# Performance work log

Measured on AMD Instinct MI355X. Metric: run time of the kernel, lower is better.

## Reference

```python
import jax, jax.numpy as jnp
import numpy as np

EMB, HEADS = 1024, 16
HEAD_DIM = EMB // HEADS


def _linear(x, W, b):
    # torch nn.Linear convention: x @ W.T + b, W: [out, in]
    return jnp.einsum('bse,oe->bso', x, W) + b


def setup_inputs() -> dict:
    key = jax.random.key(0)
    ks = jax.random.split(key, 11)
    B, S = 2, 2048
    sc = 1.0 / np.sqrt(EMB)
    inp = {
        'x': jax.random.normal(ks[0], (B, S, EMB), dtype=jnp.float32),
        'y': jax.random.normal(ks[1], (B, S, EMB), dtype=jnp.float32),
        'mask': jnp.ones((B, S, S), dtype=jnp.int32),
        'Wq': jax.random.normal(ks[2], (EMB, EMB), dtype=jnp.float32) * sc,
        'bq': jax.random.normal(ks[3], (EMB,), dtype=jnp.float32) * sc,
        'Wk': jax.random.normal(ks[4], (EMB, EMB), dtype=jnp.float32) * sc,
        'bk': jax.random.normal(ks[5], (EMB,), dtype=jnp.float32) * sc,
        'Wv': jax.random.normal(ks[6], (EMB, EMB), dtype=jnp.float32) * sc,
        'bv': jax.random.normal(ks[7], (EMB,), dtype=jnp.float32) * sc,
        'Wo': jax.random.normal(ks[8], (EMB, EMB), dtype=jnp.float32) * sc,
        'bo': jax.random.normal(ks[9], (EMB,), dtype=jnp.float32) * sc,
    }
    return inp


def reference(x, y, mask, Wq, bq, Wk, bk, Wv, bv, Wo, bo):
    B, S, _ = x.shape
    q = _linear(x, Wq, bq).reshape(B, S, HEADS, HEAD_DIM).transpose(0, 2, 1, 3)
    k = _linear(y, Wk, bk).reshape(B, -1, HEADS, HEAD_DIM).transpose(0, 2, 1, 3)
    v = _linear(y, Wv, bv).reshape(B, -1, HEADS, HEAD_DIM).transpose(0, 2, 1, 3)
    # scores: [B, H, Sq, Sk]
    score = jnp.einsum('bhqd,bhkd->bhqk', q, k) / jnp.sqrt(jnp.float32(HEAD_DIM))
    # NOTE: original torch code calls score.masked_fill(...) without assignment,
    # so the mask has no effect on the computation (faithfully ignored here).
    weights = jax.nn.softmax(score, axis=-1)
    attn = jnp.einsum('bhqk,bhkd->bhqd', weights, v)
    attn = attn.transpose(0, 2, 1, 3).reshape(B, S, EMB)
    # dropout is identity in eval mode
    return _linear(attn, Wo, bo)
```

## Files before the change

kernel.cpp:

```cpp
#include <hip/hip_runtime.h>
#include <cstdint>
#include <cstddef>

#define BB 2
#define SS 2048
#define EE 1024
#define HH 16
#define DD 64

typedef __attribute__((ext_vector_type(8))) short short8;
typedef __attribute__((ext_vector_type(4))) short shortx4;
typedef __attribute__((ext_vector_type(8))) unsigned short ushort8;
typedef __attribute__((ext_vector_type(4))) unsigned short ush4;
typedef __attribute__((ext_vector_type(4))) float floatx4;

#define MFMA32(a, b, c) __builtin_amdgcn_mfma_f32_16x16x32_bf16((a), (b), (c), 0, 0, 0)
#define MFMA16(a, b, c) __builtin_amdgcn_mfma_f32_16x16x16bf16_1k((a), (b), (c), 0, 0, 0)

#define QSCALE 0.18033688011112042f

#define G2L16(g, l)                                                        \
    __builtin_amdgcn_global_load_lds(                                      \
        (const __attribute__((address_space(1))) void*)(g),                \
        (__attribute__((address_space(3))) void*)(l), 16, 0, 0)

__device__ __forceinline__ unsigned short f2bf(float f) {
    unsigned int u = __float_as_uint(f);
    u += 0x7fffu + ((u >> 16) & 1u);
    return (unsigned short)(u >> 16);
}

__device__ __forceinline__ unsigned int pkbf(float a, float b) {
    return __builtin_amdgcn_perm(__float_as_uint(b) + 0x8000u,
                                 __float_as_uint(a) + 0x8000u, 0x07060302u);
}

__global__ __launch_bounds__(256) void k_cvt(
    const float* __restrict__ x, unsigned short* __restrict__ xb,
    const float* __restrict__ y, unsigned short* __restrict__ yb,
    const float* __restrict__ w0, unsigned short* __restrict__ d0,
    const float* __restrict__ w1, unsigned short* __restrict__ d1,
    const float* __restrict__ w2, unsigned short* __restrict__ d2,
    const float* __restrict__ w3, unsigned short* __restrict__ d3)
{
    const int g = blockIdx.y;
    if (g >= 2 && blockIdx.x >= 256) return;
    const float* s = (g == 0) ? x : (g == 1) ? y : (g == 2) ? w0
                   : (g == 3) ? w1 : (g == 4) ? w2 : w3;
    unsigned short* d = (g == 0) ? xb : (g == 1) ? yb : (g == 2) ? d0
                      : (g == 3) ? d1 : (g == 4) ? d2 : d3;
    const size_t i = ((size_t)blockIdx.x * 256 + threadIdx.x) * 16;
    floatx4 f0 = *(const floatx4*)(s + i);
    floatx4 f1 = *(const floatx4*)(s + i + 4);
    floatx4 f2 = *(const floatx4*)(s + i + 8);
    floatx4 f3 = *(const floatx4*)(s + i + 12);
    ushort8 o0, o1;
#pragma unroll
    for (int j = 0; j < 4; ++j) { o0[j] = f2bf(f0[j]); o0[j + 4] = f2bf(f1[j]); }
#pragma unroll
    for (int j = 0; j < 4; ++j) { o1[j] = f2bf(f2[j]); o1[j + 4] = f2bf(f3[j]); }
    *(ushort8*)(d + i) = o0;
    *(ushort8*)(d + i + 8) = o1;
}

template <int MT, int OMODE>
__device__ __forceinline__ void gemm_body(
    const unsigned short* __restrict__ A, const unsigned short* __restrict__ W,
    const float* __restrict__ bias, void* __restrict__ Cv, float oscale,
    int m0, int n0, unsigned short* As0, unsigned short* As1,
    unsigned short* Bs0, unsigned short* Bs1)
{
    constexpr int K = 1024, N = 1024, LDT = 32;
    constexpr int MFR = MT / 32;
    const int t = threadIdx.x;
    const int lane = t & 63, w = t >> 6;
    const int q = lane >> 4, c = lane & 15;
    const int wm = w & 1, wn = w >> 1;
    const int lr = lane >> 2, lc = (lane & 3) * 8;

    const unsigned short* gA0 = A + (size_t)(m0 + w * (MT / 4) + lr) * K + lc;
    const unsigned short* gA1 = gA0 + 16 * K;
    unsigned short* lA0_0 = As0 + (w * (MT / 4)) * LDT;
    unsigned short* lA0_1 = lA0_0 + 16 * LDT;
    unsigned short* lA1_0 = As1 + (w * (MT / 4)) * LDT;
    unsigned short* lA1_1 = lA1_0 + 16 * LDT;
    const unsigned short* gB0 = W + (size_t)(n0 + w * 32 + lr) * K + lc;
    const unsigned short* gB1 = gB0 + 16 * K;
    unsigned short* lB0_0 = Bs0 + (w * 32) * LDT;
    unsigned short* lB0_1 = lB0_0 + 16 * LDT;
    unsigned short* lB1_0 = Bs1 + (w * 32) * LDT;
    unsigned short* lB1_1 = lB1_0 + 16 * LDT;

    floatx4 acc[MFR][4] = {};

    for (int kt = 0; kt < K; kt += 64) {
        __syncthreads();
        G2L16(gA0 + kt, lA0_0);
        if constexpr (MT == 128) G2L16(gA1 + kt, lA0_1);
        G2L16(gA0 + kt + 32, lA1_0);
        if constexpr (MT == 128) G2L16(gA1 + kt + 32, lA1_1);
        G2L16(gB0 + kt, lB0_0);
        G2L16(gB1 + kt, lB0_1);
        G2L16(gB0 + kt + 32, lB1_0);
        G2L16(gB1 + kt + 32, lB1_1);
        __syncthreads();

        const unsigned short* Ah[2] = {As0, As1};
        const unsigned short* Bh[2] = {Bs0, Bs1};
#pragma unroll
        for (int hf = 0; hf < 2; ++hf) {
            short8 af[MFR], bfr[4];
#pragma unroll
            for (int mi = 0; mi < MFR; ++mi)
                af[mi] = *(const short8*)
                    &Ah[hf][(wm * (MFR * 16) + mi * 16 + c) * LDT + q * 8];
#pragma unroll
            for (int ni = 0; ni < 4; ++ni)
                bfr[ni] = *(const short8*)
                    &Bh[hf][(wn * 64 + ni * 16 + c) * LDT + q * 8];
#pragma unroll
            for (int mi = 0; mi < MFR; ++mi)
#pragma unroll
                for (int ni = 0; ni < 4; ++ni)
                    acc[mi][ni] = MFMA32(af[mi], bfr[ni], acc[mi][ni]);
        }
    }

#pragma unroll
    for (int ni = 0; ni < 4; ++ni) {
        const int col = n0 + wn * 64 + ni * 16 + c;
        const float bv = bias[col];
#pragma unroll
        for (int mi = 0; mi < MFR; ++mi)
#pragma unroll
            for (int r = 0; r < 4; ++r) {
                const int row = m0 + wm * (MFR * 16) + mi * 16 + q * 4 + r;
                const float v = (acc[mi][ni][r] + bv) * oscale;
                if constexpr (OMODE == 0) {
                    ((unsigned short*)Cv)[(size_t)row * N + col] = f2bf(v);
                } else if constexpr (OMODE == 1) {
                    const int b = row >> 11, s = row & 2047;
                    ((unsigned short*)Cv)[((size_t)(b * 1024 + col)) * SS + s] = f2bf(v);
                } else {
                    ((float*)Cv)[(size_t)row * N + col] = v;
                }
            }
    }
}

__global__ __launch_bounds__(256) void k_gemm_qkv(
    const unsigned short* __restrict__ x, const unsigned short* __restrict__ y,
    const unsigned short* __restrict__ Wq, const float* __restrict__ bq,
    const unsigned short* __restrict__ Wk, const float* __restrict__ bk,
    const unsigned short* __restrict__ Wv, const float* __restrict__ bv,
    unsigned short* __restrict__ Q, unsigned short* __restrict__ Ko,
    unsigned short* __restrict__ Vt)
{
    __shared__ __align__(16) unsigned short As0[128 * 32], As1[128 * 32];
    __shared__ __align__(16) unsigned short Bs0[128 * 32], Bs1[128 * 32];
    const int m0 = blockIdx.y * 128;
    const int nt = blockIdx.x;
    const int g = nt >> 3;
    const int n0 = (nt & 7) * 128;
    if (g == 0) {
        gemm_body<128, 0>(x, Wq, bq, Q, QSCALE, m0, n0, As0, As1, Bs0, Bs1);
    } else if (g == 1) {
        gemm_body<128, 0>(y, Wk, bk, Ko, 1.0f, m0, n0, As0, As1, Bs0, Bs1);
    } else {
        gemm_body<128, 1>(y, Wv, bv, Vt, 1.0f, m0, n0, As0, As1, Bs0, Bs1);
    }
}

__global__ __launch_bounds__(256) void k_gemm_out(
    const unsigned short* __restrict__ A, const unsigned short* __restrict__ W,
    const float* __restrict__ bias, float* __restrict__ C)
{
    __shared__ __align__(16) unsigned short As0[64 * 32], As1[64 * 32];
    __shared__ __align__(16) unsigned short Bs0[128 * 32], Bs1[128 * 32];
    gemm_body<64, 2>(A, W, bias, C, 1.0f, blockIdx.y * 64, blockIdx.x * 128,
                     As0, As1, Bs0, Bs1);
}

__global__ __launch_bounds__(256, 2) void k_attn(
    const unsigned short* __restrict__ Q, const unsigned short* __restrict__ K,
    const unsigned short* __restrict__ Vt, unsigned short* __restrict__ O)
{
    constexpr int LDK = 72;
    __shared__ __align__(16) unsigned short Ks[64 * LDK];
    __shared__ __align__(16) unsigned short Vs[64 * 64];

    const int bh = blockIdx.x, qt = blockIdx.y;
    const int b = bh >> 4, h = bh & 15;
    const int t = threadIdx.x, w = t >> 6;
    const int lane = t & 63, q = lane >> 4, c = lane & 15;

    short8 qb[2][2];
#pragma unroll
    for (int g = 0; g < 2; ++g) {
        const size_t qoff =
            (size_t)(b * SS + qt * 128 + w * 32 + g * 16 + c) * EE + h * DD + q * 8;
        qb[g][0] = *(const short8*)(Q + qoff);
        qb[g][1] = *(const short8*)(Q + qoff + 32);
    }

    floatx4 o[2][4] = {};
    floatx4 lacc[2] = {};
    const shortx4 ones = {(short)0x3F80, (short)0x3F80, (short)0x3F80, (short)0x3F80};

    const int sr = t >> 2, sp = (t & 3) * 16;
    const int vkey = (sr & 15) << 2;
    const unsigned short* Kg = K + (size_t)(b * SS + sr) * EE + h * DD + sp;
    const unsigned short* Vg = Vt + ((size_t)bh * DD + sr) * SS + sp;

    for (int kt = 0; kt < SS; kt += 64) {
        __syncthreads();
        {
            const ushort8* gk = (const ushort8*)(Kg + (size_t)kt * EE);
            ushort8 k0 = gk[0], k1 = gk[1];
            *(ushort8*)&Ks[sr * LDK + sp] = k0;
            *(ushort8*)&Ks[sr * LDK + sp + 8] = k1;
            const ushort8* gv = (const ushort8*)(Vg + kt);
            ushort8 v0 = gv[0], v1 = gv[1];
            *(ush4*)&Vs[sr * 64 + ((sp +  0) ^ vkey)] =
                __builtin_shufflevector(v0, v0, 0, 1, 2, 3);
            *(ush4*)&Vs[sr * 64 + ((sp +  4) ^ vkey)] =
                __builtin_shufflevector(v0, v0, 4, 5, 6, 7);
            *(ush4*)&Vs[sr * 64 + ((sp +  8) ^ vkey)] =
                __builtin_shufflevector(v1, v1, 0, 1, 2, 3);
            *(ush4*)&Vs[sr * 64 + ((sp + 12) ^ vkey)] =
                __builtin_shufflevector(v1, v1, 4, 5, 6, 7);
        }
        __syncthreads();

        shortx4 pa[2][4];
#pragma unroll
        for (int tt = 0; tt < 4; ++tt) {
            const short8 ka0 = *(const short8*)&Ks[(tt * 16 + c) * LDK + q * 8];
            const short8 ka1 = *(const short8*)&Ks[(tt * 16 + c) * LDK + 32 + q * 8];
#pragma unroll
            for (int g = 0; g < 2; ++g) {
                floatx4 s = {0.f, 0.f, 0.f, 0.f};
                s = MFMA32(ka0, qb[g][0], s);
                s = MFMA32(ka1, qb[g][1], s);
                union { unsigned int u[2]; shortx4 v; } pk;
                pk.u[0] = pkbf(exp2f(s[0]), exp2f(s[1]));
                pk.u[1] = pkbf(exp2f(s[2]), exp2f(s[3]));
                pa[g][tt] = pk.v;
            }
        }

#pragma unroll
        for (int nd = 0; nd < 4; ++nd)
#pragma unroll
            for (int tt = 0; tt < 4; ++tt) {
                const shortx4 vb = *(const shortx4*)
                    &Vs[(nd * 16 + c) * 64 + (((tt * 4 + q) ^ c) << 2)];
                o[0][nd] = MFMA16(pa[0][tt], vb, o[0][nd]);
                o[1][nd] = MFMA16(pa[1][tt], vb, o[1][nd]);
            }
#pragma unroll
        for (int tt = 0; tt < 4; ++tt) {
            lacc[0] = MFMA16(pa[0][tt], ones, lacc[0]);
            lacc[1] = MFMA16(pa[1][tt], ones, lacc[1]);
        }
    }

#pragma unroll
    for (int g = 0; g < 2; ++g) {
        float linv[4];
#pragma unroll
        for (int r = 0; r < 4; ++r) linv[r] = __builtin_amdgcn_rcpf(lacc[g][r]);
        const int orow = b * SS + qt * 128 + w * 32 + g * 16;
#pragma unroll
        for (int nd = 0; nd < 4; ++nd)
#pragma unroll
            for (int r = 0; r < 4; ++r)
                O[(size_t)(orow + q * 4 + r) * EE + h * DD + nd * 16 + c] =
                    f2bf(o[g][nd][r] * linv[r]);
    }
}

extern "C" void kernel_launch(void* const* d_in, const int* in_sizes, int n_in,
                              void* d_out, int out_size, void* d_ws, size_t ws_size,
                              hipStream_t stream)
{
    const float* x  = (const float*)d_in[0];
    const float* y  = (const float*)d_in[1];
    const float* Wq = (const float*)d_in[3];
    const float* bq = (const float*)d_in[4];
    const float* Wk = (const float*)d_in[5];
    const float* bk = (const float*)d_in[6];
    const float* Wv = (const float*)d_in[7];
    const float* bv = (const float*)d_in[8];
    const float* Wo = (const float*)d_in[9];
    const float* bo = (const float*)d_in[10];
    float* out = (float*)d_out;

    char* ws = (char*)d_ws;
    const size_t SZ = (size_t)BB * SS * EE * sizeof(unsigned short);
    const size_t WZ = (size_t)EE * EE * sizeof(unsigned short);
    unsigned short* xb  = (unsigned short*)(ws);
    unsigned short* yb  = (unsigned short*)(ws + SZ);
    unsigned short* Wqb = (unsigned short*)(ws + 2 * SZ);
    unsigned short* Wkb = (unsigned short*)(ws + 2 * SZ + WZ);
    unsigned short* Wvb = (unsigned short*)(ws + 2 * SZ + 2 * WZ);
    unsigned short* Wob = (unsigned short*)(ws + 2 * SZ + 3 * WZ);
    unsigned short* Qw  = (unsigned short*)(ws + 2 * SZ + 4 * WZ);
    unsigned short* Kw  = (unsigned short*)(ws + 3 * SZ + 4 * WZ);
    unsigned short* Vtw = (unsigned short*)(ws + 4 * SZ + 4 * WZ);
    unsigned short* Aw  = (unsigned short*)(ws + 5 * SZ + 4 * WZ);
    (void)ws_size; (void)in_sizes; (void)n_in; (void)out_size;

    k_cvt<<<dim3(1024, 6), 256, 0, stream>>>(x, xb, y, yb, Wq, Wqb, Wk, Wkb,
                                             Wv, Wvb, Wo, Wob);
    k_gemm_qkv<<<dim3(24, 32), 256, 0, stream>>>(xb, yb, Wqb, bq, Wkb, bk, Wvb, bv,
                                                 Qw, Kw, Vtw);
    k_attn<<<dim3(32, 16), 256, 0, stream>>>(Qw, Kw, Vtw, Aw);
    k_gemm_out<<<dim3(8, 64), 256, 0, stream>>>(Aw, Wob, bo, out);
}
```

Baseline: 245.1 us.

## Split attention key range across two wave groups and reduce via LDS

Doubles the attention block to 512 threads, with two groups of four waves each processing half of the key sequence using separate LDS tiles. The partial output accumulators and row sums from the second group are written to shared memory and added by the first group before normalization and store. This doubles the waves per CU and halves each wave's serial loop to improve latency hiding. It adds a final LDS reduction and tighter register limits from the launch bounds, which risks spills.

```diff
diff --git a/kernel.cpp b/kernel.cpp
--- a/kernel.cpp
+++ b/kernel.cpp
@@ -181,24 +181,31 @@
                      As0, As1, Bs0, Bs1);
 }
 
-__global__ __launch_bounds__(256, 2) void k_attn(
+__global__ __launch_bounds__(512, 4) void k_attn(
     const unsigned short* __restrict__ Q, const unsigned short* __restrict__ K,
     const unsigned short* __restrict__ Vt, unsigned short* __restrict__ O)
 {
     constexpr int LDK = 72;
-    __shared__ __align__(16) unsigned short Ks[64 * LDK];
-    __shared__ __align__(16) unsigned short Vs[64 * 64];
+    __shared__ __align__(16) char smem[34816];
+    unsigned short* Ksb = (unsigned short*)smem;
+    unsigned short* Vsb = (unsigned short*)(smem + 2 * 64 * LDK * 2);
+    float* Ob = (float*)smem;
 
     const int bh = blockIdx.x, qt = blockIdx.y;
     const int b = bh >> 4, h = bh & 15;
     const int t = threadIdx.x, w = t >> 6;
+    const int ws = w >> 2;
+    const int wq = w & 3;
     const int lane = t & 63, q = lane >> 4, c = lane & 15;
+
+    unsigned short* Ks = Ksb + ws * (64 * LDK);
+    unsigned short* Vs = Vsb + ws * (64 * 64);
 
     short8 qb[2][2];
 #pragma unroll
     for (int g = 0; g < 2; ++g) {
         const size_t qoff =
-            (size_t)(b * SS + qt * 128 + w * 32 + g * 16 + c) * EE + h * DD + q * 8;
+            (size_t)(b * SS + qt * 128 + wq * 32 + g * 16 + c) * EE + h * DD + q * 8;
         qb[g][0] = *(const short8*)(Q + qoff);
         qb[g][1] = *(const short8*)(Q + qoff + 32);
     }
@@ -207,12 +214,15 @@
     floatx4 lacc[2] = {};
     const shortx4 ones = {(short)0x3F80, (short)0x3F80, (short)0x3F80, (short)0x3F80};
 
-    const int sr = t >> 2, sp = (t & 3) * 16;
+    const int ts = t & 255;
+    const int sr = ts >> 2, sp = (ts & 3) * 16;
     const int vkey = (sr & 15) << 2;
-    const unsigned short* Kg = K + (size_t)(b * SS + sr) * EE + h * DD + sp;
-    const unsigned short* Vg = Vt + ((size_t)bh * DD + sr) * SS + sp;
-
-    for (int kt = 0; kt < SS; kt += 64) {
+    const unsigned short* Kg =
+        K + (size_t)(b * SS + ws * 1024 + sr) * EE + h * DD + sp;
+    const unsigned short* Vg =
+        Vt + ((size_t)bh * DD + sr) * SS + ws * 1024 + sp;
+
+    for (int kt = 0; kt < 1024; kt += 64) {
         __syncthreads();
         {
             const ushort8* gk = (const ushort8*)(Kg + (size_t)kt * EE);
@@ -265,18 +275,44 @@
         }
     }
 
-#pragma unroll
-    for (int g = 0; g < 2; ++g) {
-        float linv[4];
-#pragma unroll
-        for (int r = 0; r < 4; ++r) linv[r] = __builtin_amdgcn_rcpf(lacc[g][r]);
-        const int orow = b * SS + qt * 128 + w * 32 + g * 16;
-#pragma unroll
-        for (int nd = 0; nd < 4; ++nd)
-#pragma unroll
-            for (int r = 0; r < 4; ++r)
-                O[(size_t)(orow + q * 4 + r) * EE + h * DD + nd * 16 + c] =
-                    f2bf(o[g][nd][r] * linv[r]);
+    __syncthreads();
+    if (ws == 1) {
+#pragma unroll
+        for (int g = 0; g < 2; ++g) {
+#pragma unroll
+            for (int nd = 0; nd < 4; ++nd)
+#pragma unroll
+                for (int r = 0; r < 4; ++r)
+                    Ob[(wq * 32 + g * 16 + q * 4 + r) * 66 + nd * 16 + c] =
+                        o[g][nd][r];
+            if (c == 0) {
+#pragma unroll
+                for (int r = 0; r < 4; ++r)
+                    Ob[(wq * 32 + g * 16 + q * 4 + r) * 66 + 64] = lacc[g][r];
+            }
+        }
+    }
+    __syncthreads();
+    if (ws == 0) {
+#pragma unroll
+        for (int g = 0; g < 2; ++g) {
+            float linv[4];
+#pragma unroll
+            for (int r = 0; r < 4; ++r) {
+                const int rr = wq * 32 + g * 16 + q * 4 + r;
+#pragma unroll
+                for (int nd = 0; nd < 4; ++nd)
+                    o[g][nd][r] += Ob[rr * 66 + nd * 16 + c];
+                linv[r] = __builtin_amdgcn_rcpf(lacc[g][r] + Ob[rr * 66 + 64]);
+            }
+            const int orow = b * SS + qt * 128 + wq * 32 + g * 16;
+#pragma unroll
+            for (int nd = 0; nd < 4; ++nd)
+#pragma unroll
+                for (int r = 0; r < 4; ++r)
+                    O[(size_t)(orow + q * 4 + r) * EE + h * DD + nd * 16 + c] =
+                        f2bf(o[g][nd][r] * linv[r]);
+        }
     }
 }
 
@@ -315,6 +351,6 @@
                                              Wv, Wvb, Wo, Wob);
     k_gemm_qkv<<<dim3(24, 32), 256, 0, stream>>>(xb, yb, Wqb, bq, Wkb, bk, Wvb, bv,
                                                  Qw, Kw, Vtw);
-    k_attn<<<dim3(32, 16), 256, 0, stream>>>(Qw, Kw, Vtw, Aw);
+    k_attn<<<dim3(32, 16), 512, 0, stream>>>(Qw, Kw, Vtw, Aw);
     k_gemm_out<<<dim3(8, 64), 256, 0, stream>>>(Aw, Wob, bo, out);
 }
```

Measured after the change: 244.0 us. Within noise of the previous version (-0.5%).
